# Kernel tuning notes

Measured on AMD Instinct MI355X. Metric: run time of the kernel, lower is better.

The kernel has to match this reference:

```python
import jax, jax.numpy as jnp
import numpy as np
import math

HEAD_DIM = 64
EMBED_DIM = 512
B, T = 16, 2048

def setup_inputs() -> dict:
    key = jax.random.key(0)
    k1, k2, k3 = jax.random.split(key, 3)
    x = jax.random.normal(k1, (B, T, EMBED_DIM), dtype=jnp.float32)
    # nn.Linear-style init scale
    s = 1.0 / math.sqrt(EMBED_DIM)
    Wq = jax.random.uniform(k2, (EMBED_DIM, HEAD_DIM), dtype=jnp.float32, minval=-s, maxval=s)
    bq = jax.random.uniform(k3, (HEAD_DIM,), dtype=jnp.float32, minval=-s, maxval=s)
    return {"x": x, "Wq": Wq, "bq": bq}

def reference(x, Wq, bq):
    # Faithful to source: q, k, v all come from the SAME query projection.
    q = jnp.einsum('bte,ed->btd', x, Wq) + bq  # [B,T,D]
    d_k = q.shape[-1]
    # weights[b, i, j] = q_i . q_j / sqrt(d_k)
    weights = jnp.einsum('bid,bjd->bij', q, q) / jnp.sqrt(jnp.float32(d_k))
    # NOTE: source applies softmax over dim=1 (query/row axis), not dim=-1.
    weights = jax.nn.softmax(weights, axis=1)
    attention = jnp.einsum('bij,bjd->bid', weights, q)  # v == q in source
    return attention
```

## Files before the change

### kernel.cpp

```cpp
#include <hip/hip_runtime.h>
#include <hip/hip_bf16.h>

#define BN 16
#define TN 2048
#define DN 64
#define EN 512
#define PAD 68

using f32x4  = __attribute__((ext_vector_type(4))) float;
using bf16x8 = __attribute__((ext_vector_type(8))) short;
using bf16x4 = __attribute__((ext_vector_type(4))) short;

static __device__ __forceinline__ short f2bf(float f) {
    __hip_bfloat16 h = __float2bfloat16(f);
    return __builtin_bit_cast(short, h);
}
static __device__ __forceinline__ float bf2f(short s) {
    return __bfloat162float(__builtin_bit_cast(__hip_bfloat16, s));
}

__global__ __launch_bounds__(256) void wprep_kernel(
    const float* __restrict__ Wq, short* __restrict__ WTh,
    short* __restrict__ WTl)
{
    __shared__ float wlds[64][65];
    const int tid = threadIdx.x;
    const int k0 = blockIdx.x * 64;
    #pragma unroll
    for (int it = 0; it < 16; ++it) {
        int idx = it * 256 + tid;
        int k = idx >> 6, n = idx & 63;
        wlds[k][n] = Wq[(size_t)(k0 + k) * 64 + n];
    }
    __syncthreads();
    #pragma unroll
    for (int it = 0; it < 16; ++it) {
        int idx = it * 256 + tid;
        int n = idx >> 6, k = idx & 63;
        float v = wlds[k][n];
        short h = f2bf(v);
        short l = f2bf(v - bf2f(h));
        WTh[(size_t)n * EN + k0 + k] = h;
        WTl[(size_t)n * EN + k0 + k] = l;
    }
}

__global__ __launch_bounds__(256, 2) void qproj_kernel(
    const float* __restrict__ x, const short* __restrict__ WTh,
    const short* __restrict__ WTl, const float* __restrict__ bq,
    short* __restrict__ Qb, short* __restrict__ QTb)
{
    __shared__ short xh[64 * 40];
    __shared__ short wth[64 * 40];
    __shared__ short wtl[64 * 40];
    __shared__ short tl[64][68];

    const int tid = threadIdx.x;
    const int lane = tid & 63;
    const int wv = tid >> 6;
    const int c = lane & 15;
    const int g = lane >> 4;
    const int rowbase = blockIdx.x * 64;
    const int b = rowbase >> 11;
    const int tbase = rowbase & (TN - 1);

    const int sr = tid >> 3;
    const int sc4 = tid & 7;

    float4 xa = *reinterpret_cast<const float4*>(&x[(size_t)(rowbase + sr) * EN + sc4 * 4]);
    float4 xb = *reinterpret_cast<const float4*>(&x[(size_t)(rowbase + 32 + sr) * EN + sc4 * 4]);
    bf16x4 wa = *reinterpret_cast<const bf16x4*>(&WTh[(size_t)sr * EN + sc4 * 4]);
    bf16x4 wb = *reinterpret_cast<const bf16x4*>(&WTh[(size_t)(32 + sr) * EN + sc4 * 4]);
    bf16x4 la = *reinterpret_cast<const bf16x4*>(&WTl[(size_t)sr * EN + sc4 * 4]);
    bf16x4 lb = *reinterpret_cast<const bf16x4*>(&WTl[(size_t)(32 + sr) * EN + sc4 * 4]);

    f32x4 acc[4];
    #pragma unroll
    for (int nt = 0; nt < 4; ++nt) acc[nt] = (f32x4){0.f, 0.f, 0.f, 0.f};

    for (int ks = 0; ks < EN; ks += 32) {
        __syncthreads();
        bf16x4 h0, h1;
        #pragma unroll
        for (int j = 0; j < 4; ++j) { h0[j] = f2bf(xa[j]); h1[j] = f2bf(xb[j]); }
        *reinterpret_cast<bf16x4*>(&xh[sr * 40 + sc4 * 4]) = h0;
        *reinterpret_cast<bf16x4*>(&xh[(32 + sr) * 40 + sc4 * 4]) = h1;
        *reinterpret_cast<bf16x4*>(&wth[sr * 40 + sc4 * 4]) = wa;
        *reinterpret_cast<bf16x4*>(&wth[(32 + sr) * 40 + sc4 * 4]) = wb;
        *reinterpret_cast<bf16x4*>(&wtl[sr * 40 + sc4 * 4]) = la;
        *reinterpret_cast<bf16x4*>(&wtl[(32 + sr) * 40 + sc4 * 4]) = lb;

        const int kn = (ks + 32 < EN) ? ks + 32 : ks;
        xa = *reinterpret_cast<const float4*>(&x[(size_t)(rowbase + sr) * EN + kn + sc4 * 4]);
        xb = *reinterpret_cast<const float4*>(&x[(size_t)(rowbase + 32 + sr) * EN + kn + sc4 * 4]);
        wa = *reinterpret_cast<const bf16x4*>(&WTh[(size_t)sr * EN + kn + sc4 * 4]);
        wb = *reinterpret_cast<const bf16x4*>(&WTh[(size_t)(32 + sr) * EN + kn + sc4 * 4]);
        la = *reinterpret_cast<const bf16x4*>(&WTl[(size_t)sr * EN + kn + sc4 * 4]);
        lb = *reinterpret_cast<const bf16x4*>(&WTl[(size_t)(32 + sr) * EN + kn + sc4 * 4]);
        __syncthreads();

        bf16x8 av = *reinterpret_cast<const bf16x8*>(&xh[(wv * 16 + c) * 40 + g * 8]);
        #pragma unroll
        for (int nt = 0; nt < 4; ++nt) {
            bf16x8 bh = *reinterpret_cast<const bf16x8*>(&wth[(nt * 16 + c) * 40 + g * 8]);
            bf16x8 bl = *reinterpret_cast<const bf16x8*>(&wtl[(nt * 16 + c) * 40 + g * 8]);
            acc[nt] = __builtin_amdgcn_mfma_f32_16x16x32_bf16(av, bh, acc[nt], 0, 0, 0);
            acc[nt] = __builtin_amdgcn_mfma_f32_16x16x32_bf16(av, bl, acc[nt], 0, 0, 0);
        }
    }

    __syncthreads();
    #pragma unroll
    for (int nt = 0; nt < 4; ++nt) {
        const float bias = bq[nt * 16 + c];
        #pragma unroll
        for (int r = 0; r < 4; ++r) {
            const int row = wv * 16 + g * 4 + r;
            short qb = f2bf(acc[nt][r] + bias);
            Qb[(size_t)(rowbase + row) * DN + nt * 16 + c] = qb;
            tl[nt * 16 + c][row] = qb;
        }
    }
    __syncthreads();
    #pragma unroll
    for (int it = 0; it < 4; ++it) {
        int idx = it * 256 + tid;
        int d = idx >> 4;
        int j4 = (idx & 15) * 4;
        *reinterpret_cast<short4*>(&QTb[((size_t)(b * 64 + d)) * TN + tbase + j4]) =
            *reinterpret_cast<const short4*>(&tl[d][j4]);
    }
}

__global__ __launch_bounds__(256, 4) void stats_kernel(
    const short* __restrict__ Qb, float* __restrict__ l_part)
{
    __shared__ short Qt[64 * PAD];
    const int tid = threadIdx.x;
    const int lane = tid & 63;
    const int wv = tid >> 6;
    const int c = lane & 15;
    const int g = lane >> 4;
    const int b = blockIdx.y;
    const int z = blockIdx.z;
    const int jbase = blockIdx.x * 64 + wv * 16;
    const short* Qbb = Qb + (size_t)b * TN * DN;

    bf16x8 a0 = *reinterpret_cast<const bf16x8*>(Qbb + (size_t)(jbase + c) * DN + g * 8);
    bf16x8 a1 = *reinterpret_cast<const bf16x8*>(Qbb + (size_t)(jbase + c) * DN + g * 8 + 32);

    const int srow = tid >> 2;
    const int schk = tid & 3;
    const int ilo = z * (TN / 2);

    bf16x8 v0 = *reinterpret_cast<const bf16x8*>(Qbb + (size_t)(ilo + srow) * DN + schk * 16);
    bf16x8 v1 = *reinterpret_cast<const bf16x8*>(Qbb + (size_t)(ilo + srow) * DN + schk * 16 + 8);

    float l[4] = {0.f, 0.f, 0.f, 0.f};
    for (int ii = 0; ii < TN / 2; ii += 64) {
        __syncthreads();
        *reinterpret_cast<bf16x8*>(&Qt[srow * PAD + schk * 16]) = v0;
        *reinterpret_cast<bf16x8*>(&Qt[srow * PAD + schk * 16 + 8]) = v1;
        const int in_ = ilo + ((ii + 64 < TN / 2) ? ii + 64 : ii);
        v0 = *reinterpret_cast<const bf16x8*>(Qbb + (size_t)(in_ + srow) * DN + schk * 16);
        v1 = *reinterpret_cast<const bf16x8*>(Qbb + (size_t)(in_ + srow) * DN + schk * 16 + 8);
        __syncthreads();

        #pragma unroll
        for (int it = 0; it < 4; ++it) {
            bf16x8 b0 = *reinterpret_cast<const bf16x8*>(&Qt[(it * 16 + c) * PAD + g * 8]);
            bf16x8 b1 = *reinterpret_cast<const bf16x8*>(&Qt[(it * 16 + c) * PAD + g * 8 + 32]);
            f32x4 acc = {0.f, 0.f, 0.f, 0.f};
            acc = __builtin_amdgcn_mfma_f32_16x16x32_bf16(a0, b0, acc, 0, 0, 0);
            acc = __builtin_amdgcn_mfma_f32_16x16x32_bf16(a1, b1, acc, 0, 0, 0);
            #pragma unroll
            for (int r = 0; r < 4; ++r)
                l[r] += __expf(acc[r] * 0.125f);
        }
    }
    #pragma unroll
    for (int r = 0; r < 4; ++r) {
        float v = l[r];
        v += __shfl_xor(v, 1);
        v += __shfl_xor(v, 2);
        v += __shfl_xor(v, 4);
        v += __shfl_xor(v, 8);
        l[r] = v;
    }
    if (c == 0) {
        #pragma unroll
        for (int r = 0; r < 4; ++r)
            l_part[((size_t)z * BN + b) * TN + jbase + g * 4 + r] = l[r];
    }
}

__global__ __launch_bounds__(256) void fuse_kernel(
    const short* __restrict__ QTb, const float* __restrict__ l_part,
    short* __restrict__ RT)
{
    const int idx = blockIdx.x * 256 + threadIdx.x;
    const int c8 = idx & 255;
    const int bd = idx >> 8;
    const int b = bd >> 6;
    const int j0 = c8 * 8;

    bf16x8 q = *reinterpret_cast<const bf16x8*>(&QTb[(size_t)bd * TN + j0]);
    const float* lp0 = l_part + (size_t)b * TN + j0;
    const float* lp1 = l_part + (size_t)(BN + b) * TN + j0;
    bf16x8 r;
    #pragma unroll
    for (int t = 0; t < 8; ++t)
        r[t] = f2bf(bf2f(q[t]) / (lp0[t] + lp1[t]));
    *reinterpret_cast<bf16x8*>(&RT[(size_t)bd * TN + j0]) = r;
}

__global__ __launch_bounds__(256, 4) void pv_kernel(
    const short* __restrict__ Qb, const short* __restrict__ RT,
    float* __restrict__ out0, float* __restrict__ out1)
{
    __shared__ short Qt[64 * PAD];
    __shared__ short RTt[64 * PAD];
    __shared__ short Pt[4][16 * PAD];

    const int tid = threadIdx.x;
    const int lane = tid & 63;
    const int wv = tid >> 6;
    const int c = lane & 15;
    const int g = lane >> 4;
    const int b = blockIdx.y;
    const int z = blockIdx.z;
    const int ibase = blockIdx.x * 64 + wv * 16;
    const short* Qbb = Qb + (size_t)b * TN * DN;
    const short* RTb = RT + (size_t)b * DN * TN;

    bf16x8 bi0 = *reinterpret_cast<const bf16x8*>(Qbb + (size_t)(ibase + c) * DN + g * 8);
    bf16x8 bi1 = *reinterpret_cast<const bf16x8*>(Qbb + (size_t)(ibase + c) * DN + g * 8 + 32);

    f32x4 o[4];
    #pragma unroll
    for (int dt = 0; dt < 4; ++dt) o[dt] = (f32x4){0.f, 0.f, 0.f, 0.f};

    const int srow = tid >> 2;
    const int schk = tid & 3;
    const int jlo = z * (TN / 2);

    bf16x8 vq0 = *reinterpret_cast<const bf16x8*>(Qbb + (size_t)(jlo + srow) * DN + schk * 16);
    bf16x8 vq1 = *reinterpret_cast<const bf16x8*>(Qbb + (size_t)(jlo + srow) * DN + schk * 16 + 8);
    bf16x8 vt0 = *reinterpret_cast<const bf16x8*>(RTb + (size_t)srow * TN + jlo + schk * 16);
    bf16x8 vt1 = *reinterpret_cast<const bf16x8*>(RTb + (size_t)srow * TN + jlo + schk * 16 + 8);

    for (int jj = 0; jj < TN / 2; jj += 64) {
        __syncthreads();
        *reinterpret_cast<bf16x8*>(&Qt[srow * PAD + schk * 16]) = vq0;
        *reinterpret_cast<bf16x8*>(&Qt[srow * PAD + schk * 16 + 8]) = vq1;
        *reinterpret_cast<bf16x8*>(&RTt[srow * PAD + schk * 16]) = vt0;
        *reinterpret_cast<bf16x8*>(&RTt[srow * PAD + schk * 16 + 8]) = vt1;

        const int jn = jlo + ((jj + 64 < TN / 2) ? jj + 64 : jj);
        vq0 = *reinterpret_cast<const bf16x8*>(Qbb + (size_t)(jn + srow) * DN + schk * 16);
        vq1 = *reinterpret_cast<const bf16x8*>(Qbb + (size_t)(jn + srow) * DN + schk * 16 + 8);
        vt0 = *reinterpret_cast<const bf16x8*>(RTb + (size_t)srow * TN + jn + schk * 16);
        vt1 = *reinterpret_cast<const bf16x8*>(RTb + (size_t)srow * TN + jn + schk * 16 + 8);
        __syncthreads();

        bf16x8 aq[4][2];
        #pragma unroll
        for (int dt = 0; dt < 4; ++dt) {
            aq[dt][0] = *reinterpret_cast<const bf16x8*>(&RTt[(dt * 16 + c) * PAD + g * 8]);
            aq[dt][1] = *reinterpret_cast<const bf16x8*>(&RTt[(dt * 16 + c) * PAD + 32 + g * 8]);
        }

        #pragma unroll
        for (int jt = 0; jt < 4; ++jt) {
            bf16x8 a0 = *reinterpret_cast<const bf16x8*>(&Qt[(jt * 16 + c) * PAD + g * 8]);
            bf16x8 a1 = *reinterpret_cast<const bf16x8*>(&Qt[(jt * 16 + c) * PAD + g * 8 + 32]);
            f32x4 accs = {0.f, 0.f, 0.f, 0.f};
            accs = __builtin_amdgcn_mfma_f32_16x16x32_bf16(a0, bi0, accs, 0, 0, 0);
            accs = __builtin_amdgcn_mfma_f32_16x16x32_bf16(a1, bi1, accs, 0, 0, 0);
            bf16x4 pw;
            #pragma unroll
            for (int r = 0; r < 4; ++r)
                pw[r] = f2bf(__expf(accs[r] * 0.125f));
            *reinterpret_cast<bf16x4*>(&Pt[wv][c * PAD + jt * 16 + g * 4]) = pw;
        }
        asm volatile("s_waitcnt lgkmcnt(0)" ::: "memory");
        __builtin_amdgcn_sched_barrier(0);

        bf16x8 p0 = *reinterpret_cast<const bf16x8*>(&Pt[wv][c * PAD + g * 8]);
        bf16x8 p1 = *reinterpret_cast<const bf16x8*>(&Pt[wv][c * PAD + 32 + g * 8]);
        #pragma unroll
        for (int dt = 0; dt < 4; ++dt) {
            o[dt] = __builtin_amdgcn_mfma_f32_16x16x32_bf16(aq[dt][0], p0, o[dt], 0, 0, 0);
            o[dt] = __builtin_amdgcn_mfma_f32_16x16x32_bf16(aq[dt][1], p1, o[dt], 0, 0, 0);
        }
    }

    float* outb = (z ? out1 : out0) + (size_t)b * TN * DN;
    #pragma unroll
    for (int dt = 0; dt < 4; ++dt) {
        float4 v4;
        v4.x = o[dt][0]; v4.y = o[dt][1]; v4.z = o[dt][2]; v4.w = o[dt][3];
        *reinterpret_cast<float4*>(&outb[(size_t)(ibase + c) * DN + dt * 16 + g * 4]) = v4;
    }
}

__global__ __launch_bounds__(256) void reduce_kernel(
    float* __restrict__ out, const float* __restrict__ part1)
{
    const size_t i = (size_t)blockIdx.x * 256 + threadIdx.x;
    float4 a = reinterpret_cast<float4*>(out)[i];
    float4 b = reinterpret_cast<const float4*>(part1)[i];
    a.x += b.x; a.y += b.y; a.z += b.z; a.w += b.w;
    reinterpret_cast<float4*>(out)[i] = a;
}

extern "C" void kernel_launch(void* const* d_in, const int* in_sizes, int n_in,
                              void* d_out, int out_size, void* d_ws, size_t ws_size,
                              hipStream_t stream) {
    const float* x  = (const float*)d_in[0];
    const float* Wq = (const float*)d_in[1];
    const float* bq = (const float*)d_in[2];
    float* out = (float*)d_out;

    short* Qb   = (short*)d_ws;
    short* QTb  = Qb + (size_t)BN * TN * DN;
    short* RT   = QTb + (size_t)BN * TN * DN;
    float* lpar = (float*)(RT + (size_t)BN * TN * DN);
    short* WTh  = (short*)(lpar + (size_t)2 * BN * TN);
    short* WTl  = WTh + (size_t)DN * EN;
    float* part1 = (float*)(WTl + (size_t)DN * EN);

    wprep_kernel<<<dim3(EN / 64), dim3(256), 0, stream>>>(Wq, WTh, WTl);
    qproj_kernel<<<dim3(BN * TN / 64), dim3(256), 0, stream>>>(x, WTh, WTl, bq, Qb, QTb);
    stats_kernel<<<dim3(TN / 64, BN, 2), dim3(256), 0, stream>>>(Qb, lpar);
    fuse_kernel<<<dim3(BN * DN * TN / 8 / 256), dim3(256), 0, stream>>>(QTb, lpar, RT);
    pv_kernel<<<dim3(TN / 64, BN, 2), dim3(256), 0, stream>>>(Qb, RT, out, part1);
    reduce_kernel<<<dim3(BN * TN * DN / 4 / 256), dim3(256), 0, stream>>>(out, part1);
}
```

Measured before the change: 82.49 us.

## Split stats kernel four ways and double per-wave query rows in PV kernel

The stats kernel now splits the row-sum reduction over four i-ranges instead of two, giving more blocks and shorter loops, and the fuse kernel sums four partial denominators. The PV kernel gives each wave 32 query rows instead of 16, so each block covers 128 rows and every LDS tile of Q and R^T is reused across twice the work. The cost is more registers per thread, with launch bounds relaxed to 2 blocks per CU, fewer PV blocks, and extra partial-sum memory and traffic.

```diff
diff --git a/kernel.cpp b/kernel.cpp
--- a/kernel.cpp
+++ b/kernel.cpp
@@ -151,17 +151,17 @@
 
     const int srow = tid >> 2;
     const int schk = tid & 3;
-    const int ilo = z * (TN / 2);
+    const int ilo = z * (TN / 4);
 
     bf16x8 v0 = *reinterpret_cast<const bf16x8*>(Qbb + (size_t)(ilo + srow) * DN + schk * 16);
     bf16x8 v1 = *reinterpret_cast<const bf16x8*>(Qbb + (size_t)(ilo + srow) * DN + schk * 16 + 8);
 
     float l[4] = {0.f, 0.f, 0.f, 0.f};
-    for (int ii = 0; ii < TN / 2; ii += 64) {
+    for (int ii = 0; ii < TN / 4; ii += 64) {
         __syncthreads();
         *reinterpret_cast<bf16x8*>(&Qt[srow * PAD + schk * 16]) = v0;
         *reinterpret_cast<bf16x8*>(&Qt[srow * PAD + schk * 16 + 8]) = v1;
-        const int in_ = ilo + ((ii + 64 < TN / 2) ? ii + 64 : ii);
+        const int in_ = ilo + ((ii + 64 < TN / 4) ? ii + 64 : ii);
         v0 = *reinterpret_cast<const bf16x8*>(Qbb + (size_t)(in_ + srow) * DN + schk * 16);
         v1 = *reinterpret_cast<const bf16x8*>(Qbb + (size_t)(in_ + srow) * DN + schk * 16 + 8);
         __syncthreads();
@@ -207,20 +207,22 @@
     bf16x8 q = *reinterpret_cast<const bf16x8*>(&QTb[(size_t)bd * TN + j0]);
     const float* lp0 = l_part + (size_t)b * TN + j0;
     const float* lp1 = l_part + (size_t)(BN + b) * TN + j0;
+    const float* lp2 = l_part + (size_t)(2 * BN + b) * TN + j0;
+    const float* lp3 = l_part + (size_t)(3 * BN + b) * TN + j0;
     bf16x8 r;
     #pragma unroll
     for (int t = 0; t < 8; ++t)
-        r[t] = f2bf(bf2f(q[t]) / (lp0[t] + lp1[t]));
+        r[t] = f2bf(bf2f(q[t]) / (lp0[t] + lp1[t] + lp2[t] + lp3[t]));
     *reinterpret_cast<bf16x8*>(&RT[(size_t)bd * TN + j0]) = r;
 }
 
-__global__ __launch_bounds__(256, 4) void pv_kernel(
+__global__ __launch_bounds__(256, 2) void pv_kernel(
     const short* __restrict__ Qb, const short* __restrict__ RT,
     float* __restrict__ out0, float* __restrict__ out1)
 {
     __shared__ short Qt[64 * PAD];
     __shared__ short RTt[64 * PAD];
-    __shared__ short Pt[4][16 * PAD];
+    __shared__ short Pt[8][16 * PAD];
 
     const int tid = threadIdx.x;
     const int lane = tid & 63;
@@ -229,16 +231,24 @@
     const int g = lane >> 4;
     const int b = blockIdx.y;
     const int z = blockIdx.z;
-    const int ibase = blockIdx.x * 64 + wv * 16;
+    const int ibase = blockIdx.x * 128 + wv * 32;
     const short* Qbb = Qb + (size_t)b * TN * DN;
     const short* RTb = RT + (size_t)b * DN * TN;
 
-    bf16x8 bi0 = *reinterpret_cast<const bf16x8*>(Qbb + (size_t)(ibase + c) * DN + g * 8);
-    bf16x8 bi1 = *reinterpret_cast<const bf16x8*>(Qbb + (size_t)(ibase + c) * DN + g * 8 + 32);
-
-    f32x4 o[4];
-    #pragma unroll
-    for (int dt = 0; dt < 4; ++dt) o[dt] = (f32x4){0.f, 0.f, 0.f, 0.f};
+    bf16x8 bi[2][2];
+    #pragma unroll
+    for (int ih = 0; ih < 2; ++ih) {
+        const short* p = Qbb + (size_t)(ibase + ih * 16 + c) * DN + g * 8;
+        bi[ih][0] = *reinterpret_cast<const bf16x8*>(p);
+        bi[ih][1] = *reinterpret_cast<const bf16x8*>(p + 32);
+    }
+
+    f32x4 o[4][2];
+    #pragma unroll
+    for (int dt = 0; dt < 4; ++dt)
+        #pragma unroll
+        for (int ih = 0; ih < 2; ++ih)
+            o[dt][ih] = (f32x4){0.f, 0.f, 0.f, 0.f};
 
     const int srow = tid >> 2;
     const int schk = tid & 3;
@@ -274,33 +284,44 @@
         for (int jt = 0; jt < 4; ++jt) {
             bf16x8 a0 = *reinterpret_cast<const bf16x8*>(&Qt[(jt * 16 + c) * PAD + g * 8]);
             bf16x8 a1 = *reinterpret_cast<const bf16x8*>(&Qt[(jt * 16 + c) * PAD + g * 8 + 32]);
-            f32x4 accs = {0.f, 0.f, 0.f, 0.f};
-            accs = __builtin_amdgcn_mfma_f32_16x16x32_bf16(a0, bi0, accs, 0, 0, 0);
-            accs = __builtin_amdgcn_mfma_f32_16x16x32_bf16(a1, bi1, accs, 0, 0, 0);
-            bf16x4 pw;
             #pragma unroll
-            for (int r = 0; r < 4; ++r)
-                pw[r] = f2bf(__expf(accs[r] * 0.125f));
-            *reinterpret_cast<bf16x4*>(&Pt[wv][c * PAD + jt * 16 + g * 4]) = pw;
+            for (int ih = 0; ih < 2; ++ih) {
+                f32x4 accs = {0.f, 0.f, 0.f, 0.f};
+                accs = __builtin_amdgcn_mfma_f32_16x16x32_bf16(a0, bi[ih][0], accs, 0, 0, 0);
+                accs = __builtin_amdgcn_mfma_f32_16x16x32_bf16(a1, bi[ih][1], accs, 0, 0, 0);
+                bf16x4 pw;
+                #pragma unroll
+                for (int r = 0; r < 4; ++r)
+                    pw[r] = f2bf(__expf(accs[r] * 0.125f));
+                *reinterpret_cast<bf16x4*>(&Pt[wv * 2 + ih][c * PAD + jt * 16 + g * 4]) = pw;
+            }
         }
         asm volatile("s_waitcnt lgkmcnt(0)" ::: "memory");
         __builtin_amdgcn_sched_barrier(0);
 
-        bf16x8 p0 = *reinterpret_cast<const bf16x8*>(&Pt[wv][c * PAD + g * 8]);
-        bf16x8 p1 = *reinterpret_cast<const bf16x8*>(&Pt[wv][c * PAD + 32 + g * 8]);
-        #pragma unroll
-        for (int dt = 0; dt < 4; ++dt) {
-            o[dt] = __builtin_amdgcn_mfma_f32_16x16x32_bf16(aq[dt][0], p0, o[dt], 0, 0, 0);
-            o[dt] = __builtin_amdgcn_mfma_f32_16x16x32_bf16(aq[dt][1], p1, o[dt], 0, 0, 0);
+        #pragma unroll
+        for (int ih = 0; ih < 2; ++ih) {
+            bf16x8 p0 = *reinterpret_cast<const bf16x8*>(&Pt[wv * 2 + ih][c * PAD + g * 8]);
+            bf16x8 p1 = *reinterpret_cast<const bf16x8*>(&Pt[wv * 2 + ih][c * PAD + 32 + g * 8]);
+            #pragma unroll
+            for (int dt = 0; dt < 4; ++dt) {
+                o[dt][ih] = __builtin_amdgcn_mfma_f32_16x16x32_bf16(aq[dt][0], p0, o[dt][ih], 0, 0, 0);
+                o[dt][ih] = __builtin_amdgcn_mfma_f32_16x16x32_bf16(aq[dt][1], p1, o[dt][ih], 0, 0, 0);
+            }
         }
     }
 
     float* outb = (z ? out1 : out0) + (size_t)b * TN * DN;
     #pragma unroll
     for (int dt = 0; dt < 4; ++dt) {
-        float4 v4;
-        v4.x = o[dt][0]; v4.y = o[dt][1]; v4.z = o[dt][2]; v4.w = o[dt][3];
-        *reinterpret_cast<float4*>(&outb[(size_t)(ibase + c) * DN + dt * 16 + g * 4]) = v4;
+        #pragma unroll
+        for (int ih = 0; ih < 2; ++ih) {
+            float4 v4;
+            v4.x = o[dt][ih][0]; v4.y = o[dt][ih][1];
+            v4.z = o[dt][ih][2]; v4.w = o[dt][ih][3];
+            *reinterpret_cast<float4*>(
+                &outb[(size_t)(ibase + ih * 16 + c) * DN + dt * 16 + g * 4]) = v4;
+        }
     }
 }
 
@@ -326,14 +347,14 @@
     short* QTb  = Qb + (size_t)BN * TN * DN;
     short* RT   = QTb + (size_t)BN * TN * DN;
     float* lpar = (float*)(RT + (size_t)BN * TN * DN);
-    short* WTh  = (short*)(lpar + (size_t)2 * BN * TN);
+    short* WTh  = (short*)(lpar + (size_t)4 * BN * TN);
     short* WTl  = WTh + (size_t)DN * EN;
     float* part1 = (float*)(WTl + (size_t)DN * EN);
 
     wprep_kernel<<<dim3(EN / 64), dim3(256), 0, stream>>>(Wq, WTh, WTl);
     qproj_kernel<<<dim3(BN * TN / 64), dim3(256), 0, stream>>>(x, WTh, WTl, bq, Qb, QTb);
-    stats_kernel<<<dim3(TN / 64, BN, 2), dim3(256), 0, stream>>>(Qb, lpar);
+    stats_kernel<<<dim3(TN / 64, BN, 4), dim3(256), 0, stream>>>(Qb, lpar);
     fuse_kernel<<<dim3(BN * DN * TN / 8 / 256), dim3(256), 0, stream>>>(QTb, lpar, RT);
-    pv_kernel<<<dim3(TN / 64, BN, 2), dim3(256), 0, stream>>>(Qb, RT, out, part1);
+    pv_kernel<<<dim3(TN / 128, BN, 2), dim3(256), 0, stream>>>(Qb, RT, out, part1);
     reduce_kernel<<<dim3(BN * TN * DN / 4 / 256), dim3(256), 0, stream>>>(out, part1);
 }
```

New measurement: 79.22 us. 1.04x faster.
